# Kernel optimization log

Measured on AMD Instinct MI355X. Metric: run time of the kernel, lower is better.

The kernel has to match this reference:

```python
import jax, jax.numpy as jnp
import numpy as np

N_NODES = 40000
N_EDGES = 640000
NUM_GRAPHS = 64
NODE_DIM = 128
EDGE_DIM = 32
HID = 64
AGG_HID = 128
NEG_SLOPE = 0.2


def _segment_softmax(logits, seg, num_segments):
    # logits: [E, H], seg: [E] target-node index. Numerically stable per-segment softmax.
    m = jax.ops.segment_max(logits, seg, num_segments=num_segments)
    m = jnp.where(jnp.isfinite(m), m, 0.0)  # empty segments -> -inf max
    e = jnp.exp(logits - m[seg])
    denom = jax.ops.segment_sum(e, seg, num_segments=num_segments)
    return e / (denom[seg] + 1e-16)


def gatv2_conv(x, edge_index, edge_attr, Wl, bl, Wr, br, We, att, bias, concat):
    # PyG GATv2Conv with edge features (share_weights=False, lin_edge bias-free).
    N = x.shape[0]
    H, C = att.shape
    src, dst = edge_index[0], edge_index[1]
    xl = (x @ Wl + bl).reshape(N, H, C)          # lin_l(x) -> source transform
    xr = (x @ Wr + br).reshape(N, H, C)          # lin_r(x) -> target transform
    ee = (edge_attr @ We).reshape(-1, H, C)       # lin_edge(edge_attr)
    m = jax.nn.leaky_relu(xl[src] + xr[dst] + ee, NEG_SLOPE)  # [E,H,C]
    logits = jnp.einsum('ehc,hc->eh', m, att)     # [E,H]
    alpha = _segment_softmax(logits, dst, N)      # softmax over incoming edges
    out = jax.ops.segment_sum(xl[src] * alpha[..., None], dst, num_segments=N)  # [N,H,C]
    out = out.reshape(N, H * C) if concat else out.mean(axis=1)
    return out + bias


def setup_inputs() -> dict:
    key = jax.random.key(0)
    ks = iter(jax.random.split(key, 40))
    rn = lambda shape, s=0.1: (jax.random.normal(next(ks), shape, dtype=jnp.float32) * s)
    inp = {}
    inp['x'] = jax.random.normal(next(ks), (N_NODES, NODE_DIM), dtype=jnp.float32)
    inp['edge_attr'] = jax.random.normal(next(ks), (N_EDGES, EDGE_DIM), dtype=jnp.float32)
    inp['edge_index'] = jax.random.randint(next(ks), (2, N_EDGES), 0, N_NODES, dtype=jnp.int32)
    inp['batch'] = jnp.sort(jax.random.randint(next(ks), (N_NODES,), 0, NUM_GRAPHS, dtype=jnp.int32))
    inp.update(W1l=rn((NODE_DIM, 2 * HID)), b1l=jnp.zeros((2 * HID,), jnp.float32),
               W1r=rn((NODE_DIM, 2 * HID)), b1r=jnp.zeros((2 * HID,), jnp.float32),
               W1e=rn((EDGE_DIM, 2 * HID)), att1=rn((2, HID)), bias1=jnp.zeros((2 * HID,), jnp.float32))
    inp.update(W2l=rn((2 * HID, 2 * HID)), b2l=jnp.zeros((2 * HID,), jnp.float32),
               W2r=rn((2 * HID, 2 * HID)), b2r=jnp.zeros((2 * HID,), jnp.float32),
               W2e=rn((EDGE_DIM, 2 * HID)), att2=rn((2, HID)), bias2=jnp.zeros((2 * HID,), jnp.float32))
    # conv3: 128 -> 64, 1 head, concat=False
    inp.update(W3l=rn((2 * HID, HID)), b3l=jnp.zeros((HID,), jnp.float32),
               W3r=rn((2 * HID, HID)), b3r=jnp.zeros((HID,), jnp.float32),
               W3e=rn((EDGE_DIM, HID)), att3=rn((1, HID)), bias3=jnp.zeros((HID,), jnp.float32))
    inp.update(G1w=rn((HID, AGG_HID)), G1b=jnp.zeros((AGG_HID,), jnp.float32),
               G2w=rn((AGG_HID, 1)), G2b=jnp.zeros((1,), jnp.float32),
               Wreg=rn((HID, 1)), breg=jnp.zeros((1,), jnp.float32))
    return inp


def reference(x, edge_attr, edge_index, batch,
              W1l, b1l, W1r, b1r, W1e, att1, bias1,
              W2l, b2l, W2r, b2r, W2e, att2, bias2,
              W3l, b3l, W3r, b3r, W3e, att3, bias3,
              G1w, G1b, G2w, G2b, Wreg, breg):
    h = jax.nn.relu(gatv2_conv(x, edge_index, edge_attr, W1l, b1l, W1r, b1r, W1e, att1, bias1, True))
    h = jax.nn.relu(gatv2_conv(h, edge_index, edge_attr, W2l, b2l, W2r, b2r, W2e, att2, bias2, True))
    h = gatv2_conv(h, edge_index, edge_attr, W3l, b3l, W3r, b3r, W3e, att3, bias3, False)  # [N, HID]
    # Attentional aggregation over nodes, per graph
    gate = (jax.nn.relu(h @ G1w + G1b) @ G2w + G2b)[:, 0]            # [N]
    gate = _segment_softmax(gate[:, None], batch, NUM_GRAPHS)[:, 0]   # softmax within each graph
    pooled = jax.ops.segment_sum(gate[:, None] * h, batch, num_segments=NUM_GRAPHS)  # [B, HID]
    return (pooled @ Wreg + breg).squeeze(-1)  # [B]
```

## Files before the change

kernel.cpp:

```cpp
#include <hip/hip_runtime.h>

__global__ void k_fill(unsigned* p, int n, unsigned v) {
    int i = blockIdx.x * blockDim.x + threadIdx.x;
    if (i < n) p[i] = v;
}

__global__ void k_hist(const int* __restrict__ ei, int E, int* __restrict__ deg) {
    int e = blockIdx.x * blockDim.x + threadIdx.x;
    if (e < E) atomicAdd(&deg[ei[E + e]], 1);
}

__global__ void k_scan_blocks(const int* __restrict__ deg, int N,
                              int* __restrict__ excl, int* __restrict__ parts) {
    __shared__ int s[256];
    int t = threadIdx.x, i = blockIdx.x * 256 + t;
    int v = (i < N) ? deg[i] : 0;
    s[t] = v;
    __syncthreads();
    int acc = v;
    for (int off = 1; off < 256; off <<= 1) {
        int add = (t >= off) ? s[t - off] : 0;
        __syncthreads();
        acc += add;
        s[t] = acc;
        __syncthreads();
    }
    if (i < N) excl[i] = acc - v;
    if (t == 255) parts[blockIdx.x] = acc;
}

__global__ void k_scan_parts(int* __restrict__ parts, int nb) {
    __shared__ int s[256];
    int t = threadIdx.x;
    int v = (t < nb) ? parts[t] : 0;
    s[t] = v;
    __syncthreads();
    int acc = v;
    for (int off = 1; off < 256; off <<= 1) {
        int add = (t >= off) ? s[t - off] : 0;
        __syncthreads();
        acc += add;
        s[t] = acc;
        __syncthreads();
    }
    if (t < nb) parts[t] = acc - v;
}

__global__ void k_scan_add(const int* __restrict__ excl, const int* __restrict__ parts,
                           int* __restrict__ row_ptr, int* __restrict__ cursor, int N) {
    int i = blockIdx.x * blockDim.x + threadIdx.x;
    if (i >= N) return;
    int r = excl[i] + parts[i >> 8];
    row_ptr[i] = r;
    cursor[i] = r;
}

__global__ void k_scatter(const int* __restrict__ ei, int E, int* __restrict__ cursor,
                          int2* __restrict__ elist) {
    int e = blockIdx.x * blockDim.x + threadIdx.x;
    if (e >= E) return;
    int d = ei[E + e];
    int j = atomicAdd(&cursor[d], 1);
    elist[j] = make_int2(ei[e], e);
}

__global__ void k_reorder(const int2* __restrict__ elist, const float* __restrict__ ea, int E,
                          float4* __restrict__ ea_s) {
    int idx = blockIdx.x * blockDim.x + threadIdx.x;
    int j = idx >> 3, q = idx & 7;
    if (j >= E) return;
    ea_s[(size_t)j * 8 + q] = ((const float4*)ea)[(size_t)elist[j].y * 8 + q];
}

template <int M, int RW>
__global__ __launch_bounds__(256) void k_gemm2(const float* __restrict__ A,
                                               const float* __restrict__ Wl, const float* __restrict__ bl,
                                               const float* __restrict__ Wr, const float* __restrict__ br,
                                               float* __restrict__ outl, float* __restrict__ outr) {
    constexpr int TX = M / 4;
    __shared__ float sA[32][68];
    __shared__ float sW[32][M];
    const float* W    = blockIdx.y ? Wr : Wl;
    const float* bias = blockIdx.y ? br : bl;
    float* out        = blockIdx.y ? outr : outl;
    int t = threadIdx.x;
    int tx = t % TX, ty = t / TX;
    int r0 = blockIdx.x * 64;
    float acc[RW][4] = {};
    for (int kt = 0; kt < 128; kt += 32) {
        for (int l = t; l < 512; l += 256) {
            int row = l >> 3, kq = (l & 7) << 2;
            float4 a = *(const float4*)&A[(size_t)(r0 + row) * 128 + kt + kq];
            sA[kq + 0][row] = a.x; sA[kq + 1][row] = a.y;
            sA[kq + 2][row] = a.z; sA[kq + 3][row] = a.w;
        }
        for (int l = t; l < 32 * M / 4; l += 256) {
            int kk = (l * 4) / M, cc = (l * 4) % M;
            *(float4*)&sW[kk][cc] = *(const float4*)&W[(size_t)(kt + kk) * M + cc];
        }
        __syncthreads();
#pragma unroll
        for (int k = 0; k < 32; k++) {
            float4 w = *(float4*)&sW[k][tx * 4];
            float ar[RW];
#pragma unroll
            for (int i = 0; i < RW; i += 4) {
                float4 a = *(float4*)&sA[k][ty * RW + i];
                ar[i] = a.x; ar[i + 1] = a.y; ar[i + 2] = a.z; ar[i + 3] = a.w;
            }
#pragma unroll
            for (int i = 0; i < RW; i++) {
                acc[i][0] += ar[i] * w.x; acc[i][1] += ar[i] * w.y;
                acc[i][2] += ar[i] * w.z; acc[i][3] += ar[i] * w.w;
            }
        }
        __syncthreads();
    }
    float4 b = *(const float4*)&bias[tx * 4];
#pragma unroll
    for (int i = 0; i < RW; i++) {
        float4 v;
        v.x = acc[i][0] + b.x; v.y = acc[i][1] + b.y;
        v.z = acc[i][2] + b.z; v.w = acc[i][3] + b.w;
        *(float4*)&out[(size_t)(r0 + ty * RW + i) * M + tx * 4] = v;
    }
}

template <int H, bool RELU, bool SORTED>
__global__ __launch_bounds__(256) void k_agg(const float* __restrict__ xl, const float* __restrict__ xr,
                                             const float* __restrict__ ea, const float4* __restrict__ ea_s,
                                             const int2* __restrict__ elist,
                                             const int* __restrict__ row_ptr, const int* __restrict__ deg,
                                             const float* __restrict__ We, const float* __restrict__ att,
                                             const float* __restrict__ bias, float* __restrict__ out, int N) {
    constexpr int HC = H * 64;
    int tid = threadIdx.x, wv = tid >> 6, lane = tid & 63;
    float rWe0[32], rWe1[H == 2 ? 32 : 1];
#pragma unroll
    for (int k = 0; k < 32; k++) rWe0[k] = We[k * HC + lane];
    if constexpr (H == 2) {
#pragma unroll
        for (int k = 0; k < 32; k++) rWe1[k] = We[k * HC + 64 + lane];
    }
    float att0 = att[lane], b0 = bias[lane];
    float att1 = 0.f, b1 = 0.f;
    if constexpr (H == 2) { att1 = att[64 + lane]; b1 = bias[64 + lane]; }
    int n = blockIdx.x * 4 + wv;
    if (n >= N) return;
    int start = row_ptr[n], d = deg[n];
    float xr0 = xr[(size_t)n * HC + lane];
    float xr1 = (H == 2) ? xr[(size_t)n * HC + 64 + lane] : 0.f;
    float acc0 = 0.f, acc1 = 0.f, den0 = 0.f, den1 = 0.f;
    for (int j = 0; j < d; j++) {
        int2 sp = elist[start + j];
        const float4* eap = SORTED ? (ea_s + (size_t)(start + j) * 8)
                                   : (const float4*)(ea + (size_t)sp.y * 32);
        const float* xls = xl + (size_t)sp.x * HC;
        float xl0 = xls[lane];
        float xl1 = (H == 2) ? xls[64 + lane] : 0.f;
        float ee0 = 0.f, ee1 = 0.f;
#pragma unroll
        for (int kq = 0; kq < 8; kq++) {
            float4 v = eap[kq];
            ee0 = fmaf(v.x, rWe0[kq * 4 + 0], ee0);
            ee0 = fmaf(v.y, rWe0[kq * 4 + 1], ee0);
            ee0 = fmaf(v.z, rWe0[kq * 4 + 2], ee0);
            ee0 = fmaf(v.w, rWe0[kq * 4 + 3], ee0);
            if constexpr (H == 2) {
                ee1 = fmaf(v.x, rWe1[kq * 4 + 0], ee1);
                ee1 = fmaf(v.y, rWe1[kq * 4 + 1], ee1);
                ee1 = fmaf(v.z, rWe1[kq * 4 + 2], ee1);
                ee1 = fmaf(v.w, rWe1[kq * 4 + 3], ee1);
            }
        }
        float v0 = xl0 + xr0 + ee0;
        v0 = v0 > 0.f ? v0 : 0.2f * v0;
        float p0 = att0 * v0, p1 = 0.f;
        if constexpr (H == 2) {
            float v1 = xl1 + xr1 + ee1;
            v1 = v1 > 0.f ? v1 : 0.2f * v1;
            p1 = att1 * v1;
        }
#pragma unroll
        for (int m = 32; m; m >>= 1) {
            p0 += __shfl_xor(p0, m);
            if constexpr (H == 2) p1 += __shfl_xor(p1, m);
        }
        float ex0 = __expf(p0);
        acc0 = fmaf(ex0, xl0, acc0);
        den0 += ex0;
        if constexpr (H == 2) {
            float ex1 = __expf(p1);
            acc1 = fmaf(ex1, xl1, acc1);
            den1 += ex1;
        }
    }
    float o0 = acc0 / (den0 + 1e-16f) + b0;
    if (RELU) o0 = o0 > 0.f ? o0 : 0.f;
    out[(size_t)n * HC + lane] = o0;
    if constexpr (H == 2) {
        float o1 = acc1 / (den1 + 1e-16f) + b1;
        if (RELU) o1 = o1 > 0.f ? o1 : 0.f;
        out[(size_t)n * HC + 64 + lane] = o1;
    }
}

__global__ __launch_bounds__(256) void k_gate(const float* __restrict__ h, const float* __restrict__ G1w,
                                              const float* __restrict__ G1b, const float* __restrict__ G2w,
                                              const float* __restrict__ G2b,
                                              float* __restrict__ gate, int N) {
    __shared__ float sH[64][64];
    __shared__ float part[64][2];
    int t = threadIdx.x;
    int n0 = blockIdx.x * 64;
    for (int l = t; l < 1024; l += 256) {
        float4 v = ((const float4*)(h + (size_t)n0 * 64))[l];
        int n = l >> 4, kq = (l & 15) << 2;
        *(float4*)&sH[n][kq] = v;
    }
    int c = t & 127, half = t >> 7;
    float rW[64];
#pragma unroll
    for (int k = 0; k < 64; k++) rW[k] = G1w[k * 128 + c];
    float g1b = G1b[c], g2w = G2w[c];
    __syncthreads();
    for (int nn = 0; nn < 32; nn++) {
        int n = half * 32 + nn;
        float acc = g1b;
#pragma unroll
        for (int k = 0; k < 64; k += 4) {
            float4 hv = *(const float4*)&sH[n][k];
            acc = fmaf(hv.x, rW[k], acc);
            acc = fmaf(hv.y, rW[k + 1], acc);
            acc = fmaf(hv.z, rW[k + 2], acc);
            acc = fmaf(hv.w, rW[k + 3], acc);
        }
        acc = acc > 0.f ? acc : 0.f;
        float p = acc * g2w;
#pragma unroll
        for (int m = 32; m; m >>= 1) p += __shfl_xor(p, m);
        if ((t & 63) == 0) part[n][(t >> 6) & 1] = p;
    }
    __syncthreads();
    if (t < 64) gate[n0 + t] = __expf(part[t][0] + part[t][1] + G2b[0]);
}

__global__ __launch_bounds__(256) void k_pool(const float* __restrict__ h, const float* __restrict__ gate,
                                              const int* __restrict__ batch,
                                              float* __restrict__ pooled, int N) {
    int g = blockIdx.x;
    int lo = 0, hi = N;
    while (lo < hi) { int mid = (lo + hi) >> 1; if (batch[mid] < g) lo = mid + 1; else hi = mid; }
    int start = lo;
    lo = 0; hi = N;
    while (lo < hi) { int mid = (lo + hi) >> 1; if (batch[mid] < g + 1) lo = mid + 1; else hi = mid; }
    int end = lo;
    int t = threadIdx.x, wv = t >> 6, lane = t & 63;
    float acc = 0.f, den = 0.f;
    for (int n = start + wv; n < end; n += 4) {
        float gv = gate[n];
        acc = fmaf(gv, h[(size_t)n * 64 + lane], acc);
        den += gv;
    }
    __shared__ float sacc[4][64];
    __shared__ float sden[4];
    sacc[wv][lane] = acc;
    if (lane == 0) sden[wv] = den;
    __syncthreads();
    if (wv == 0) {
        float a = sacc[0][lane] + sacc[1][lane] + sacc[2][lane] + sacc[3][lane];
        float d = sden[0] + sden[1] + sden[2] + sden[3] + 1e-16f;
        pooled[g * 64 + lane] = a / d;
    }
}

__global__ void k_final(const float* __restrict__ pooled, const float* __restrict__ Wreg,
                        const float* __restrict__ breg, float* __restrict__ out) {
    int g = threadIdx.x;
    float acc = breg[0];
    for (int c = 0; c < 64; c++) acc += pooled[g * 64 + c] * Wreg[c];
    out[g] = acc;
}

extern "C" void kernel_launch(void* const* d_in, const int* in_sizes, int n_in,
                              void* d_out, int out_size, void* d_ws, size_t ws_size,
                              hipStream_t stream) {
    const float* x  = (const float*)d_in[0];
    const float* ea = (const float*)d_in[1];
    const int* ei    = (const int*)d_in[2];
    const int* batch = (const int*)d_in[3];
    auto ff = [&](int i) { return (const float*)d_in[i]; };
    const float *W1l = ff(4), *b1l = ff(5), *W1r = ff(6), *b1r = ff(7), *W1e = ff(8),
                *att1 = ff(9), *bias1 = ff(10);
    const float *W2l = ff(11), *b2l = ff(12), *W2r = ff(13), *b2r = ff(14), *W2e = ff(15),
                *att2 = ff(16), *bias2 = ff(17);
    const float *W3l = ff(18), *b3l = ff(19), *W3r = ff(20), *b3r = ff(21), *W3e = ff(22),
                *att3 = ff(23), *bias3 = ff(24);
    const float *G1w = ff(25), *G1b = ff(26), *G2w = ff(27), *G2b = ff(28), *Wreg = ff(29),
                *breg = ff(30);

    const int N = in_sizes[0] / 128;
    const int E = in_sizes[2] / 2;

    char* ws = (char*)d_ws;
    float*  bufA    = (float*)(ws);
    float*  bufB    = (float*)(ws + 20480000);
    float*  bufH    = (float*)(ws + 40960000);
    int2*   elist   = (int2*)(ws + 61440000);
    int*    row_ptr = (int*)(ws + 66560000);
    int*    deg     = (int*)(ws + 66720000);
    int*    cursor  = (int*)(ws + 66880000);
    int*    excl    = (int*)(ws + 67040000);
    int*    parts   = (int*)(ws + 67200000);
    float*  gate    = (float*)(ws + 67204096);
    float*  pooled  = (float*)(ws + 67364096);
    float4* ea_s    = (float4*)(ws + 67380480);
    const bool sorted_ea = ws_size >= (size_t)67380480 + (size_t)E * 32 * 4;

    auto cdiv = [](int a, int b) { return (a + b - 1) / b; };
    const int NB = cdiv(N, 256);
    const dim3 gemmG(N / 64, 2);
    const int AGGB = cdiv(N, 4);

    k_fill<<<NB, 256, 0, stream>>>((unsigned*)deg, N, 0u);
    k_hist<<<cdiv(E, 256), 256, 0, stream>>>(ei, E, deg);
    k_scan_blocks<<<NB, 256, 0, stream>>>(deg, N, excl, parts);
    k_scan_parts<<<1, 256, 0, stream>>>(parts, NB);
    k_scan_add<<<NB, 256, 0, stream>>>(excl, parts, row_ptr, cursor, N);
    k_scatter<<<cdiv(E, 256), 256, 0, stream>>>(ei, E, cursor, elist);
    if (sorted_ea)
        k_reorder<<<cdiv(E * 8, 256), 256, 0, stream>>>(elist, ea, E, ea_s);

    k_gemm2<128, 8><<<gemmG, 256, 0, stream>>>(x, W1l, b1l, W1r, b1r, bufA, bufB);
    if (sorted_ea)
        k_agg<2, true, true><<<AGGB, 256, 0, stream>>>(bufA, bufB, ea, ea_s, elist, row_ptr, deg, W1e, att1, bias1, bufH, N);
    else
        k_agg<2, true, false><<<AGGB, 256, 0, stream>>>(bufA, bufB, ea, ea_s, elist, row_ptr, deg, W1e, att1, bias1, bufH, N);

    k_gemm2<128, 8><<<gemmG, 256, 0, stream>>>(bufH, W2l, b2l, W2r, b2r, bufA, bufB);
    if (sorted_ea)
        k_agg<2, true, true><<<AGGB, 256, 0, stream>>>(bufA, bufB, ea, ea_s, elist, row_ptr, deg, W2e, att2, bias2, bufH, N);
    else
        k_agg<2, true, false><<<AGGB, 256, 0, stream>>>(bufA, bufB, ea, ea_s, elist, row_ptr, deg, W2e, att2, bias2, bufH, N);

    k_gemm2<64, 4><<<gemmG, 256, 0, stream>>>(bufH, W3l, b3l, W3r, b3r, bufA, bufB);
    if (sorted_ea)
        k_agg<1, false, true><<<AGGB, 256, 0, stream>>>(bufA, bufB, ea, ea_s, elist, row_ptr, deg, W3e, att3, bias3, bufH, N);
    else
        k_agg<1, false, false><<<AGGB, 256, 0, stream>>>(bufA, bufB, ea, ea_s, elist, row_ptr, deg, W3e, att3, bias3, bufH, N);

    k_gate<<<N / 64, 256, 0, stream>>>(bufH, G1w, G1b, G2w, G2b, gate, N);
    k_pool<<<64, 256, 0, stream>>>(bufH, gate, batch, pooled, N);
    k_final<<<1, 64, 0, stream>>>(pooled, Wreg, breg, (float*)d_out);
}
```

Baseline: 1.065 ms.

## Remap GATv2 aggregation lanes to two columns each with edge-pair processing

Reworks the per-node aggregation kernel so each lane owns two adjacent output columns loaded as float2. For two heads, the two half-waves each take one head and process edges in pairs. For one head, the two half-waves take different edges and merge their partial sums with a cross-half shuffle at the end. This cuts register use for the edge-weight matrix, shortens shuffle reductions to 32 lanes, and adds launch bounds for two blocks per SM. The aim is more in-flight edge loads and higher occupancy, in exchange for more complex indexing and a final cross-half merge.

```diff
diff --git a/kernel.cpp b/kernel.cpp
--- a/kernel.cpp
+++ b/kernel.cpp
@@ -127,82 +127,114 @@
 }
 
 template <int H, bool RELU, bool SORTED>
-__global__ __launch_bounds__(256) void k_agg(const float* __restrict__ xl, const float* __restrict__ xr,
-                                             const float* __restrict__ ea, const float4* __restrict__ ea_s,
-                                             const int2* __restrict__ elist,
-                                             const int* __restrict__ row_ptr, const int* __restrict__ deg,
-                                             const float* __restrict__ We, const float* __restrict__ att,
-                                             const float* __restrict__ bias, float* __restrict__ out, int N) {
+__global__ __launch_bounds__(256, 2) void k_agg(const float* __restrict__ xl, const float* __restrict__ xr,
+                                                const float* __restrict__ ea, const float4* __restrict__ ea_s,
+                                                const int2* __restrict__ elist,
+                                                const int* __restrict__ row_ptr, const int* __restrict__ deg,
+                                                const float* __restrict__ We, const float* __restrict__ att,
+                                                const float* __restrict__ bias, float* __restrict__ out, int N) {
     constexpr int HC = H * 64;
     int tid = threadIdx.x, wv = tid >> 6, lane = tid & 63;
-    float rWe0[32], rWe1[H == 2 ? 32 : 1];
-#pragma unroll
-    for (int k = 0; k < 32; k++) rWe0[k] = We[k * HC + lane];
-    if constexpr (H == 2) {
-#pragma unroll
-        for (int k = 0; k < 32; k++) rWe1[k] = We[k * HC + 64 + lane];
-    }
-    float att0 = att[lane], b0 = bias[lane];
-    float att1 = 0.f, b1 = 0.f;
-    if constexpr (H == 2) { att1 = att[64 + lane]; b1 = bias[64 + lane]; }
+    int half = lane >> 5, c2 = lane & 31;
+    int col = (H == 2 ? half * 64 : 0) + 2 * c2;
     int n = blockIdx.x * 4 + wv;
     if (n >= N) return;
+
+    float2 rWe[32];
+#pragma unroll
+    for (int k = 0; k < 32; k++) rWe[k] = *(const float2*)&We[k * HC + col];
+    float2 attv = *(const float2*)&att[col];
+    float2 bv   = *(const float2*)&bias[col];
+    float2 xrv  = *(const float2*)&xr[(size_t)n * HC + col];
+
     int start = row_ptr[n], d = deg[n];
-    float xr0 = xr[(size_t)n * HC + lane];
-    float xr1 = (H == 2) ? xr[(size_t)n * HC + 64 + lane] : 0.f;
-    float acc0 = 0.f, acc1 = 0.f, den0 = 0.f, den1 = 0.f;
-    for (int j = 0; j < d; j++) {
-        int2 sp = elist[start + j];
-        const float4* eap = SORTED ? (ea_s + (size_t)(start + j) * 8)
+    float2 acc = make_float2(0.f, 0.f);
+    float den = 0.f;
+
+    auto edge_pre = [&](int slot, float2& xlv, float& p) {
+        int2 sp = elist[slot];
+        const float4* eap = SORTED ? (ea_s + (size_t)slot * 8)
                                    : (const float4*)(ea + (size_t)sp.y * 32);
-        const float* xls = xl + (size_t)sp.x * HC;
-        float xl0 = xls[lane];
-        float xl1 = (H == 2) ? xls[64 + lane] : 0.f;
-        float ee0 = 0.f, ee1 = 0.f;
+        xlv = *(const float2*)&xl[(size_t)sp.x * HC + col];
+        float2 ee = make_float2(0.f, 0.f);
 #pragma unroll
         for (int kq = 0; kq < 8; kq++) {
             float4 v = eap[kq];
-            ee0 = fmaf(v.x, rWe0[kq * 4 + 0], ee0);
-            ee0 = fmaf(v.y, rWe0[kq * 4 + 1], ee0);
-            ee0 = fmaf(v.z, rWe0[kq * 4 + 2], ee0);
-            ee0 = fmaf(v.w, rWe0[kq * 4 + 3], ee0);
-            if constexpr (H == 2) {
-                ee1 = fmaf(v.x, rWe1[kq * 4 + 0], ee1);
-                ee1 = fmaf(v.y, rWe1[kq * 4 + 1], ee1);
-                ee1 = fmaf(v.z, rWe1[kq * 4 + 2], ee1);
-                ee1 = fmaf(v.w, rWe1[kq * 4 + 3], ee1);
+            ee.x = fmaf(v.x, rWe[kq * 4 + 0].x, ee.x); ee.y = fmaf(v.x, rWe[kq * 4 + 0].y, ee.y);
+            ee.x = fmaf(v.y, rWe[kq * 4 + 1].x, ee.x); ee.y = fmaf(v.y, rWe[kq * 4 + 1].y, ee.y);
+            ee.x = fmaf(v.z, rWe[kq * 4 + 2].x, ee.x); ee.y = fmaf(v.z, rWe[kq * 4 + 2].y, ee.y);
+            ee.x = fmaf(v.w, rWe[kq * 4 + 3].x, ee.x); ee.y = fmaf(v.w, rWe[kq * 4 + 3].y, ee.y);
+        }
+        float v0 = xlv.x + xrv.x + ee.x;
+        float v1 = xlv.y + xrv.y + ee.y;
+        v0 = v0 > 0.f ? v0 : 0.2f * v0;
+        v1 = v1 > 0.f ? v1 : 0.2f * v1;
+        p = attv.x * v0 + attv.y * v1;
+    };
+
+    if constexpr (H == 2) {
+        int j = 0;
+        for (; j + 2 <= d; j += 2) {
+            float2 xla, xlb;
+            float pa, pb;
+            edge_pre(start + j, xla, pa);
+            edge_pre(start + j + 1, xlb, pb);
+#pragma unroll
+            for (int m = 16; m; m >>= 1) { pa += __shfl_xor(pa, m); pb += __shfl_xor(pb, m); }
+            float exa = __expf(pa), exb = __expf(pb);
+            acc.x = fmaf(exa, xla.x, acc.x); acc.y = fmaf(exa, xla.y, acc.y);
+            acc.x = fmaf(exb, xlb.x, acc.x); acc.y = fmaf(exb, xlb.y, acc.y);
+            den += exa + exb;
+        }
+        if (j < d) {
+            float2 xla;
+            float pa;
+            edge_pre(start + j, xla, pa);
+#pragma unroll
+            for (int m = 16; m; m >>= 1) pa += __shfl_xor(pa, m);
+            float exa = __expf(pa);
+            acc.x = fmaf(exa, xla.x, acc.x); acc.y = fmaf(exa, xla.y, acc.y);
+            den += exa;
+        }
+    } else {
+        for (int j = 0; j < d; j += 4) {
+            {
+                int jj = j + half;
+                bool valid = jj < d;
+                int slot = start + (valid ? jj : j);
+                float2 xla;
+                float pa;
+                edge_pre(slot, xla, pa);
+#pragma unroll
+                for (int m = 16; m; m >>= 1) pa += __shfl_xor(pa, m);
+                float exa = valid ? __expf(pa) : 0.f;
+                acc.x = fmaf(exa, xla.x, acc.x); acc.y = fmaf(exa, xla.y, acc.y);
+                den += exa;
             }
-        }
-        float v0 = xl0 + xr0 + ee0;
-        v0 = v0 > 0.f ? v0 : 0.2f * v0;
-        float p0 = att0 * v0, p1 = 0.f;
-        if constexpr (H == 2) {
-            float v1 = xl1 + xr1 + ee1;
-            v1 = v1 > 0.f ? v1 : 0.2f * v1;
-            p1 = att1 * v1;
-        }
-#pragma unroll
-        for (int m = 32; m; m >>= 1) {
-            p0 += __shfl_xor(p0, m);
-            if constexpr (H == 2) p1 += __shfl_xor(p1, m);
-        }
-        float ex0 = __expf(p0);
-        acc0 = fmaf(ex0, xl0, acc0);
-        den0 += ex0;
-        if constexpr (H == 2) {
-            float ex1 = __expf(p1);
-            acc1 = fmaf(ex1, xl1, acc1);
-            den1 += ex1;
-        }
-    }
-    float o0 = acc0 / (den0 + 1e-16f) + b0;
-    if (RELU) o0 = o0 > 0.f ? o0 : 0.f;
-    out[(size_t)n * HC + lane] = o0;
-    if constexpr (H == 2) {
-        float o1 = acc1 / (den1 + 1e-16f) + b1;
-        if (RELU) o1 = o1 > 0.f ? o1 : 0.f;
-        out[(size_t)n * HC + 64 + lane] = o1;
-    }
+            if (j + 2 < d) {
+                int jj = j + 2 + half;
+                bool valid = jj < d;
+                int slot = start + (valid ? jj : j);
+                float2 xlb;
+                float pb;
+                edge_pre(slot, xlb, pb);
+#pragma unroll
+                for (int m = 16; m; m >>= 1) pb += __shfl_xor(pb, m);
+                float exb = valid ? __expf(pb) : 0.f;
+                acc.x = fmaf(exb, xlb.x, acc.x); acc.y = fmaf(exb, xlb.y, acc.y);
+                den += exb;
+            }
+        }
+        acc.x += __shfl_xor(acc.x, 32);
+        acc.y += __shfl_xor(acc.y, 32);
+        den   += __shfl_xor(den, 32);
+    }
+
+    float inv = 1.f / (den + 1e-16f);
+    float o0 = acc.x * inv + bv.x;
+    float o1 = acc.y * inv + bv.y;
+    if (RELU) { o0 = fmaxf(o0, 0.f); o1 = fmaxf(o1, 0.f); }
+    *(float2*)&out[(size_t)n * HC + col] = make_float2(o0, o1);
 }
 
 __global__ __launch_bounds__(256) void k_gate(const float* __restrict__ h, const float* __restrict__ G1w,
```

After: 1.695 ms. +59.2%, slower.

## Split GATv2 aggregation across waves by head and edge parity

Applied to the files above, without the earlier changes.

The aggregation kernel now gives each wave one head and half of a node's edges (even or odd), instead of one wave handling all heads and edges of a node. The two partial softmax sums are combined through shared memory after a block barrier. This raises parallelism per node, halves the per-wave register set for the edge weights, and issues all eight edge-feature loads up front with two FMA chains for more ILP. In exchange, the edge-feature row is now loaded and multiplied by each head's wave separately, blocks shrink to 1–2 nodes, and a __syncthreads plus shared-memory exchange is added.

```diff
diff --git a/kernel.cpp b/kernel.cpp
--- a/kernel.cpp
+++ b/kernel.cpp
@@ -134,74 +134,74 @@
                                              const float* __restrict__ We, const float* __restrict__ att,
                                              const float* __restrict__ bias, float* __restrict__ out, int N) {
     constexpr int HC = H * 64;
+    __shared__ float sAcc[2][64];
+    __shared__ float sDen[2];
     int tid = threadIdx.x, wv = tid >> 6, lane = tid & 63;
-    float rWe0[32], rWe1[H == 2 ? 32 : 1];
-#pragma unroll
-    for (int k = 0; k < 32; k++) rWe0[k] = We[k * HC + lane];
+    int h, eh, n, slotIdx;
     if constexpr (H == 2) {
-#pragma unroll
-        for (int k = 0; k < 32; k++) rWe1[k] = We[k * HC + 64 + lane];
-    }
-    float att0 = att[lane], b0 = bias[lane];
-    float att1 = 0.f, b1 = 0.f;
-    if constexpr (H == 2) { att1 = att[64 + lane]; b1 = bias[64 + lane]; }
-    int n = blockIdx.x * 4 + wv;
-    if (n >= N) return;
-    int start = row_ptr[n], d = deg[n];
-    float xr0 = xr[(size_t)n * HC + lane];
-    float xr1 = (H == 2) ? xr[(size_t)n * HC + 64 + lane] : 0.f;
-    float acc0 = 0.f, acc1 = 0.f, den0 = 0.f, den1 = 0.f;
-    for (int j = 0; j < d; j++) {
-        int2 sp = elist[start + j];
-        const float4* eap = SORTED ? (ea_s + (size_t)(start + j) * 8)
+        h = wv >> 1; eh = wv & 1; n = blockIdx.x; slotIdx = h;
+    } else {
+        h = 0; eh = wv & 1; n = blockIdx.x * 2 + (wv >> 1); slotIdx = wv >> 1;
+    }
+    int col = h * 64 + lane;
+
+    float rWe[32];
+#pragma unroll
+    for (int k = 0; k < 32; k++) rWe[k] = We[k * HC + col];
+    float attv = att[col], bv = bias[col];
+
+    bool alive = n < N;
+    float xrv = 0.f;
+    int start = 0, d = 0;
+    if (alive) {
+        xrv = xr[(size_t)n * HC + col];
+        start = row_ptr[n];
+        d = deg[n];
+    }
+
+    float acc = 0.f, den = 0.f;
+    for (int j = eh; j < d; j += 2) {
+        int slot = start + j;
+        int2 sp = elist[slot];
+        const float4* eap = SORTED ? (ea_s + (size_t)slot * 8)
                                    : (const float4*)(ea + (size_t)sp.y * 32);
-        const float* xls = xl + (size_t)sp.x * HC;
-        float xl0 = xls[lane];
-        float xl1 = (H == 2) ? xls[64 + lane] : 0.f;
-        float ee0 = 0.f, ee1 = 0.f;
-#pragma unroll
-        for (int kq = 0; kq < 8; kq++) {
-            float4 v = eap[kq];
-            ee0 = fmaf(v.x, rWe0[kq * 4 + 0], ee0);
-            ee0 = fmaf(v.y, rWe0[kq * 4 + 1], ee0);
-            ee0 = fmaf(v.z, rWe0[kq * 4 + 2], ee0);
-            ee0 = fmaf(v.w, rWe0[kq * 4 + 3], ee0);
-            if constexpr (H == 2) {
-                ee1 = fmaf(v.x, rWe1[kq * 4 + 0], ee1);
-                ee1 = fmaf(v.y, rWe1[kq * 4 + 1], ee1);
-                ee1 = fmaf(v.z, rWe1[kq * 4 + 2], ee1);
-                ee1 = fmaf(v.w, rWe1[kq * 4 + 3], ee1);
-            }
-        }
-        float v0 = xl0 + xr0 + ee0;
-        v0 = v0 > 0.f ? v0 : 0.2f * v0;
-        float p0 = att0 * v0, p1 = 0.f;
-        if constexpr (H == 2) {
-            float v1 = xl1 + xr1 + ee1;
-            v1 = v1 > 0.f ? v1 : 0.2f * v1;
-            p1 = att1 * v1;
-        }
-#pragma unroll
-        for (int m = 32; m; m >>= 1) {
-            p0 += __shfl_xor(p0, m);
-            if constexpr (H == 2) p1 += __shfl_xor(p1, m);
-        }
-        float ex0 = __expf(p0);
-        acc0 = fmaf(ex0, xl0, acc0);
-        den0 += ex0;
-        if constexpr (H == 2) {
-            float ex1 = __expf(p1);
-            acc1 = fmaf(ex1, xl1, acc1);
-            den1 += ex1;
-        }
-    }
-    float o0 = acc0 / (den0 + 1e-16f) + b0;
-    if (RELU) o0 = o0 > 0.f ? o0 : 0.f;
-    out[(size_t)n * HC + lane] = o0;
-    if constexpr (H == 2) {
-        float o1 = acc1 / (den1 + 1e-16f) + b1;
-        if (RELU) o1 = o1 > 0.f ? o1 : 0.f;
-        out[(size_t)n * HC + 64 + lane] = o1;
+        float4 r[8];
+#pragma unroll
+        for (int q = 0; q < 8; q++) r[q] = eap[q];
+        float xlv = xl[(size_t)sp.x * HC + col];
+        float eeA = 0.f, eeB = 0.f;
+#pragma unroll
+        for (int q = 0; q < 8; q += 2) {
+            eeA = fmaf(r[q].x, rWe[q * 4 + 0], eeA);
+            eeA = fmaf(r[q].y, rWe[q * 4 + 1], eeA);
+            eeA = fmaf(r[q].z, rWe[q * 4 + 2], eeA);
+            eeA = fmaf(r[q].w, rWe[q * 4 + 3], eeA);
+            eeB = fmaf(r[q + 1].x, rWe[q * 4 + 4], eeB);
+            eeB = fmaf(r[q + 1].y, rWe[q * 4 + 5], eeB);
+            eeB = fmaf(r[q + 1].z, rWe[q * 4 + 6], eeB);
+            eeB = fmaf(r[q + 1].w, rWe[q * 4 + 7], eeB);
+        }
+        float v = xlv + xrv + (eeA + eeB);
+        v = v > 0.f ? v : 0.2f * v;
+        float p = attv * v;
+#pragma unroll
+        for (int m = 32; m; m >>= 1) p += __shfl_xor(p, m);
+        float ex = __expf(p);
+        acc = fmaf(ex, xlv, acc);
+        den += ex;
+    }
+
+    if (eh == 1) {
+        sAcc[slotIdx][lane] = acc;
+        if (lane == 0) sDen[slotIdx] = den;
+    }
+    __syncthreads();
+    if (eh == 0 && alive) {
+        float a = acc + sAcc[slotIdx][lane];
+        float dd = den + sDen[slotIdx] + 1e-16f;
+        float o = a / dd + bv;
+        if (RELU) o = fmaxf(o, 0.f);
+        out[(size_t)n * HC + col] = o;
     }
 }
 
@@ -320,7 +320,8 @@
     auto cdiv = [](int a, int b) { return (a + b - 1) / b; };
     const int NB = cdiv(N, 256);
     const dim3 gemmG(N / 64, 2);
-    const int AGGB = cdiv(N, 4);
+    const int AGGB2 = N;
+    const int AGGB1 = cdiv(N, 2);
 
     k_fill<<<NB, 256, 0, stream>>>((unsigned*)deg, N, 0u);
     k_hist<<<cdiv(E, 256), 256, 0, stream>>>(ei, E, deg);
@@ -333,21 +334,21 @@
 
     k_gemm2<128, 8><<<gemmG, 256, 0, stream>>>(x, W1l, b1l, W1r, b1r, bufA, bufB);
     if (sorted_ea)
-        k_agg<2, true, true><<<AGGB, 256, 0, stream>>>(bufA, bufB, ea, ea_s, elist, row_ptr, deg, W1e, att1, bias1, bufH, N);
+        k_agg<2, true, true><<<AGGB2, 256, 0, stream>>>(bufA, bufB, ea, ea_s, elist, row_ptr, deg, W1e, att1, bias1, bufH, N);
     else
-        k_agg<2, true, false><<<AGGB, 256, 0, stream>>>(bufA, bufB, ea, ea_s, elist, row_ptr, deg, W1e, att1, bias1, bufH, N);
+        k_agg<2, true, false><<<AGGB2, 256, 0, stream>>>(bufA, bufB, ea, ea_s, elist, row_ptr, deg, W1e, att1, bias1, bufH, N);
 
     k_gemm2<128, 8><<<gemmG, 256, 0, stream>>>(bufH, W2l, b2l, W2r, b2r, bufA, bufB);
     if (sorted_ea)
-        k_agg<2, true, true><<<AGGB, 256, 0, stream>>>(bufA, bufB, ea, ea_s, elist, row_ptr, deg, W2e, att2, bias2, bufH, N);
+        k_agg<2, true, true><<<AGGB2, 256, 0, stream>>>(bufA, bufB, ea, ea_s, elist, row_ptr, deg, W2e, att2, bias2, bufH, N);
     else
-        k_agg<2, true, false><<<AGGB, 256, 0, stream>>>(bufA, bufB, ea, ea_s, elist, row_ptr, deg, W2e, att2, bias2, bufH, N);
+        k_agg<2, true, false><<<AGGB2, 256, 0, stream>>>(bufA, bufB, ea, ea_s, elist, row_ptr, deg, W2e, att2, bias2, bufH, N);
 
     k_gemm2<64, 4><<<gemmG, 256, 0, stream>>>(bufH, W3l, b3l, W3r, b3r, bufA, bufB);
     if (sorted_ea)
-        k_agg<1, false, true><<<AGGB, 256, 0, stream>>>(bufA, bufB, ea, ea_s, elist, row_ptr, deg, W3e, att3, bias3, bufH, N);
+        k_agg<1, false, true><<<AGGB1, 256, 0, stream>>>(bufA, bufB, ea, ea_s, elist, row_ptr, deg, W3e, att3, bias3, bufH, N);
     else
-        k_agg<1, false, false><<<AGGB, 256, 0, stream>>>(bufA, bufB, ea, ea_s, elist, row_ptr, deg, W3e, att3, bias3, bufH, N);
+        k_agg<1, false, false><<<AGGB1, 256, 0, stream>>>(bufA, bufB, ea, ea_s, elist, row_ptr, deg, W3e, att3, bias3, bufH, N);
 
     k_gate<<<N / 64, 256, 0, stream>>>(bufH, G1w, G1b, G2w, G2b, gate, N);
     k_pool<<<64, 256, 0, stream>>>(bufH, gate, batch, pooled, N);
```

After: 1.628 ms. 1.53x slower.

## Precompute edge projections with tiled GEMM and rework aggregation with split-edge waves

Applied to the files above, without the earlier changes.

The per-edge lin_edge projection moves out of the aggregation loop into a separate shared-memory tiled GEMM. That kernel writes edge embeddings in CSR order into workspace, chunked over node ranges when the workspace is too small. A new aggregation kernel reads those precomputed embeddings, gives each lane two channels via float2, splits a node's edges between two waves and prefetches the next edge's data. The aim is to remove the redundant per-lane 32-term dot products and improve memory parallelism. The cost is a large extra write and read of E×HC floats per layer. The softmax also applies exp without subtracting a max, which could overflow for large logits.

```diff
diff --git a/kernel.cpp b/kernel.cpp
--- a/kernel.cpp
+++ b/kernel.cpp
@@ -62,14 +62,6 @@
     int d = ei[E + e];
     int j = atomicAdd(&cursor[d], 1);
     elist[j] = make_int2(ei[e], e);
-}
-
-__global__ void k_reorder(const int2* __restrict__ elist, const float* __restrict__ ea, int E,
-                          float4* __restrict__ ea_s) {
-    int idx = blockIdx.x * blockDim.x + threadIdx.x;
-    int j = idx >> 3, q = idx & 7;
-    if (j >= E) return;
-    ea_s[(size_t)j * 8 + q] = ((const float4*)ea)[(size_t)elist[j].y * 8 + q];
 }
 
 template <int M, int RW>
@@ -126,13 +118,148 @@
     }
 }
 
-template <int H, bool RELU, bool SORTED>
-__global__ __launch_bounds__(256) void k_agg(const float* __restrict__ xl, const float* __restrict__ xr,
-                                             const float* __restrict__ ea, const float4* __restrict__ ea_s,
-                                             const int2* __restrict__ elist,
-                                             const int* __restrict__ row_ptr, const int* __restrict__ deg,
-                                             const float* __restrict__ We, const float* __restrict__ att,
-                                             const float* __restrict__ bias, float* __restrict__ out, int N) {
+template <int HC>
+__global__ __launch_bounds__(256) void k_edge_gemm(const float* __restrict__ ea,
+                                                   const int2* __restrict__ elist,
+                                                   const int* __restrict__ row_ptr,
+                                                   const float* __restrict__ We,
+                                                   float* __restrict__ ee,
+                                                   int n0, int n1, int Ntot, int E) {
+    int s0 = row_ptr[n0];
+    int s1 = (n1 >= Ntot) ? E : row_ptr[n1];
+    int sb = s0 + blockIdx.x * 64;
+    if (sb >= s1) return;
+    __shared__ float sA[64][33];
+    __shared__ float sW[32][HC];
+    int t = threadIdx.x;
+    for (int l = t; l < 512; l += 256) {
+        int row = l >> 3, q = l & 7;
+        int s = sb + row;
+        int eid = (s < s1) ? elist[s].y : 0;
+        float4 a = *(const float4*)&ea[(size_t)eid * 32 + q * 4];
+        sA[row][q * 4 + 0] = a.x; sA[row][q * 4 + 1] = a.y;
+        sA[row][q * 4 + 2] = a.z; sA[row][q * 4 + 3] = a.w;
+    }
+    for (int l = t; l < 32 * HC / 4; l += 256) {
+        int k = (l * 4) / HC, c = (l * 4) % HC;
+        *(float4*)&sW[k][c] = *(const float4*)&We[k * HC + c];
+    }
+    __syncthreads();
+    constexpr int CG = HC / 4;
+    constexpr int RPT = CG / 4;
+    int tx = t % CG, ty = t / CG;
+    float acc[RPT][4] = {};
+#pragma unroll
+    for (int k = 0; k < 32; k++) {
+        float4 w = *(float4*)&sW[k][tx * 4];
+#pragma unroll
+        for (int i = 0; i < RPT; i++) {
+            float a = sA[ty * RPT + i][k];
+            acc[i][0] = fmaf(a, w.x, acc[i][0]);
+            acc[i][1] = fmaf(a, w.y, acc[i][1]);
+            acc[i][2] = fmaf(a, w.z, acc[i][2]);
+            acc[i][3] = fmaf(a, w.w, acc[i][3]);
+        }
+    }
+#pragma unroll
+    for (int i = 0; i < RPT; i++) {
+        int s = sb + ty * RPT + i;
+        if (s < s1)
+            *(float4*)&ee[(size_t)(s - s0) * HC + tx * 4] =
+                make_float4(acc[i][0], acc[i][1], acc[i][2], acc[i][3]);
+    }
+}
+
+template <int H, bool RELU>
+__global__ __launch_bounds__(256) void k_aggv(const float* __restrict__ xl, const float* __restrict__ xr,
+                                              const float* __restrict__ ee,
+                                              const int2* __restrict__ elist,
+                                              const int* __restrict__ row_ptr, const int* __restrict__ deg,
+                                              const float* __restrict__ att, const float* __restrict__ bias,
+                                              float* __restrict__ out, int n0, int n1) {
+    constexpr int HC = H * 64;
+    __shared__ float2 sAcc[2][64];
+    __shared__ float  sDen[2][64];
+    int tid = threadIdx.x, wv = tid >> 6, lane = tid & 63;
+    int ns = wv >> 1, eh = wv & 1;
+    int n = n0 + blockIdx.x * 2 + ns;
+    bool alive = n < n1;
+    int hf = lane >> 5, c2 = lane & 31;
+    int col = (H == 2) ? (hf * 64 + 2 * c2) : (2 * c2);
+    float2 attv = *(const float2*)&att[col];
+    int s0 = row_ptr[n0];
+    float2 xrv = make_float2(0.f, 0.f);
+    int start = 0, d = 0;
+    if (alive) {
+        xrv = *(const float2*)&xr[(size_t)n * HC + col];
+        start = row_ptr[n];
+        d = deg[n];
+    }
+    float2 acc = make_float2(0.f, 0.f);
+    float den = 0.f;
+
+    const int jstep = (H == 2) ? 2 : 4;
+    int jc = (H == 2) ? eh : (2 * eh + hf);
+    bool okc = jc < d;
+    int sC = start + jc;
+    int sN = sC + jstep;
+    int spx = okc ? elist[sC].x : 0;
+    float2 eeC = okc ? *(const float2*)&ee[(size_t)(sC - s0) * HC + col] : make_float2(0.f, 0.f);
+    float2 xlC = okc ? *(const float2*)&xl[(size_t)spx * HC + col] : make_float2(0.f, 0.f);
+    bool okn = (jc + jstep) < d;
+    int spxN = okn ? elist[sN].x : 0;
+
+    while (okc) {
+        bool okn2 = (jc + 2 * jstep) < d;
+        int sN2 = sN + jstep;
+        int spxN2 = okn2 ? elist[sN2].x : 0;
+        float2 eeN = okn ? *(const float2*)&ee[(size_t)(sN - s0) * HC + col] : make_float2(0.f, 0.f);
+        float2 xlN = okn ? *(const float2*)&xl[(size_t)spxN * HC + col] : make_float2(0.f, 0.f);
+
+        float v0 = xlC.x + xrv.x + eeC.x;
+        float v1 = xlC.y + xrv.y + eeC.y;
+        v0 = v0 > 0.f ? v0 : 0.2f * v0;
+        v1 = v1 > 0.f ? v1 : 0.2f * v1;
+        float p = fmaf(attv.x, v0, attv.y * v1);
+#pragma unroll
+        for (int m = 16; m; m >>= 1) p += __shfl_xor(p, m);
+        float ex = __expf(p);
+        acc.x = fmaf(ex, xlC.x, acc.x);
+        acc.y = fmaf(ex, xlC.y, acc.y);
+        den += ex;
+
+        jc += jstep; sC = sN; sN = sN2;
+        xlC = xlN; eeC = eeN; spxN = spxN2;
+        okc = okn; okn = okn2;
+    }
+
+    if constexpr (H == 1) {
+        acc.x += __shfl_xor(acc.x, 32);
+        acc.y += __shfl_xor(acc.y, 32);
+        den   += __shfl_xor(den, 32);
+    }
+    if (eh == 1) { sAcc[ns][lane] = acc; sDen[ns][lane] = den; }
+    __syncthreads();
+    if (eh == 0 && alive) {
+        float2 a = sAcc[ns][lane];
+        float dd = sDen[ns][lane];
+        float dsum = den + dd + 1e-16f;
+        float2 bv = *(const float2*)&bias[col];
+        float o0 = (acc.x + a.x) / dsum + bv.x;
+        float o1 = (acc.y + a.y) / dsum + bv.y;
+        if (RELU) { o0 = fmaxf(o0, 0.f); o1 = fmaxf(o1, 0.f); }
+        if (H == 2 || hf == 0)
+            *(float2*)&out[(size_t)n * HC + col] = make_float2(o0, o1);
+    }
+}
+
+template <int H, bool RELU>
+__global__ __launch_bounds__(256) void k_agg_fb(const float* __restrict__ xl, const float* __restrict__ xr,
+                                                const float* __restrict__ ea,
+                                                const int2* __restrict__ elist,
+                                                const int* __restrict__ row_ptr, const int* __restrict__ deg,
+                                                const float* __restrict__ We, const float* __restrict__ att,
+                                                const float* __restrict__ bias, float* __restrict__ out, int N) {
     constexpr int HC = H * 64;
     int tid = threadIdx.x, wv = tid >> 6, lane = tid & 63;
     float rWe0[32], rWe1[H == 2 ? 32 : 1];
@@ -153,8 +280,7 @@
     float acc0 = 0.f, acc1 = 0.f, den0 = 0.f, den1 = 0.f;
     for (int j = 0; j < d; j++) {
         int2 sp = elist[start + j];
-        const float4* eap = SORTED ? (ea_s + (size_t)(start + j) * 8)
-                                   : (const float4*)(ea + (size_t)sp.y * 32);
+        const float4* eap = (const float4*)(ea + (size_t)sp.y * 32);
         const float* xls = xl + (size_t)sp.x * HC;
         float xl0 = xls[lane];
         float xl1 = (H == 2) ? xls[64 + lane] : 0.f;
@@ -282,6 +408,26 @@
     out[g] = acc;
 }
 
+template <int H, bool RELU>
+static void launch_layer_agg(const float* ea, const int2* elist, const int* row_ptr, const int* deg,
+                             const float* We, const float* att, const float* bias,
+                             const float* xl, const float* xr, float* outb, float* eebuf,
+                             size_t avail, int N, int E, hipStream_t stream) {
+    constexpr int HC = H * 64;
+    size_t need = (size_t)E * HC * 4;
+    int K = (avail >= need) ? 1 : (int)((need * 21 / 20 + avail - 1) / avail);
+    size_t cap_slots = (K == 1) ? (size_t)E : avail / ((size_t)HC * 4);
+    size_t cover = cap_slots < (size_t)E ? cap_slots : (size_t)E;
+    int gb = (int)((cover + 63) / 64);
+    for (int c = 0; c < K; c++) {
+        int n0 = (int)((long long)N * c / K);
+        int n1 = (int)((long long)N * (c + 1) / K);
+        k_edge_gemm<HC><<<gb, 256, 0, stream>>>(ea, elist, row_ptr, We, eebuf, n0, n1, N, E);
+        int nb = (n1 - n0 + 1) / 2;
+        k_aggv<H, RELU><<<nb, 256, 0, stream>>>(xl, xr, eebuf, elist, row_ptr, deg, att, bias, outb, n0, n1);
+    }
+}
+
 extern "C" void kernel_launch(void* const* d_in, const int* in_sizes, int n_in,
                               void* d_out, int out_size, void* d_ws, size_t ws_size,
                               hipStream_t stream) {
@@ -314,13 +460,13 @@
     int*    parts   = (int*)(ws + 67200000);
     float*  gate    = (float*)(ws + 67204096);
     float*  pooled  = (float*)(ws + 67364096);
-    float4* ea_s    = (float4*)(ws + 67380480);
-    const bool sorted_ea = ws_size >= (size_t)67380480 + (size_t)E * 32 * 4;
+    float*  eebuf   = (float*)(ws + 67380480);
+    size_t avail = ws_size > (size_t)67380480 ? ws_size - (size_t)67380480 : 0;
+    const bool newpath = avail >= ((size_t)64 << 20);
 
     auto cdiv = [](int a, int b) { return (a + b - 1) / b; };
     const int NB = cdiv(N, 256);
     const dim3 gemmG(N / 64, 2);
-    const int AGGB = cdiv(N, 4);
 
     k_fill<<<NB, 256, 0, stream>>>((unsigned*)deg, N, 0u);
     k_hist<<<cdiv(E, 256), 256, 0, stream>>>(ei, E, deg);
@@ -328,26 +474,23 @@
     k_scan_parts<<<1, 256, 0, stream>>>(parts, NB);
     k_scan_add<<<NB, 256, 0, stream>>>(excl, parts, row_ptr, cursor, N);
     k_scatter<<<cdiv(E, 256), 256, 0, stream>>>(ei, E, cursor, elist);
-    if (sorted_ea)
-        k_reorder<<<cdiv(E * 8, 256), 256, 0, stream>>>(elist, ea, E, ea_s);
-
-    k_gemm2<128, 8><<<gemmG, 256, 0, stream>>>(x, W1l, b1l, W1r, b1r, bufA, bufB);
-    if (sorted_ea)
-        k_agg<2, true, true><<<AGGB, 256, 0, stream>>>(bufA, bufB, ea, ea_s, elist, row_ptr, deg, W1e, att1, bias1, bufH, N);
-    else
-        k_agg<2, true, false><<<AGGB, 256, 0, stream>>>(bufA, bufB, ea, ea_s, elist, row_ptr, deg, W1e, att1, bias1, bufH, N);
-
-    k_gemm2<128, 8><<<gemmG, 256, 0, stream>>>(bufH, W2l, b2l, W2r, b2r, bufA, bufB);
-    if (sorted_ea)
-        k_agg<2, true, true><<<AGGB, 256, 0, stream>>>(bufA, bufB, ea, ea_s, elist, row_ptr, deg, W2e, att2, bias2, bufH, N);
-    else
-        k_agg<2, true, false><<<AGGB, 256, 0, stream>>>(bufA, bufB, ea, ea_s, elist, row_ptr, deg, W2e, att2, bias2, bufH, N);
-
-    k_gemm2<64, 4><<<gemmG, 256, 0, stream>>>(bufH, W3l, b3l, W3r, b3r, bufA, bufB);
-    if (sorted_ea)
-        k_agg<1, false, true><<<AGGB, 256, 0, stream>>>(bufA, bufB, ea, ea_s, elist, row_ptr, deg, W3e, att3, bias3, bufH, N);
-    else
-        k_agg<1, false, false><<<AGGB, 256, 0, stream>>>(bufA, bufB, ea, ea_s, elist, row_ptr, deg, W3e, att3, bias3, bufH, N);
+
+    if (newpath) {
+        k_gemm2<128, 8><<<gemmG, 256, 0, stream>>>(x, W1l, b1l, W1r, b1r, bufA, bufB);
+        launch_layer_agg<2, true>(ea, elist, row_ptr, deg, W1e, att1, bias1, bufA, bufB, bufH, eebuf, avail, N, E, stream);
+        k_gemm2<128, 8><<<gemmG, 256, 0, stream>>>(bufH, W2l, b2l, W2r, b2r, bufA, bufB);
+        launch_layer_agg<2, true>(ea, elist, row_ptr, deg, W2e, att2, bias2, bufA, bufB, bufH, eebuf, avail, N, E, stream);
+        k_gemm2<64, 4><<<gemmG, 256, 0, stream>>>(bufH, W3l, b3l, W3r, b3r, bufA, bufB);
+        launch_layer_agg<1, false>(ea, elist, row_ptr, deg, W3e, att3, bias3, bufA, bufB, bufH, eebuf, avail, N, E, stream);
+    } else {
+        const int AGGB = cdiv(N, 4);
+        k_gemm2<128, 8><<<gemmG, 256, 0, stream>>>(x, W1l, b1l, W1r, b1r, bufA, bufB);
+        k_agg_fb<2, true><<<AGGB, 256, 0, stream>>>(bufA, bufB, ea, elist, row_ptr, deg, W1e, att1, bias1, bufH, N);
+        k_gemm2<128, 8><<<gemmG, 256, 0, stream>>>(bufH, W2l, b2l, W2r, b2r, bufA, bufB);
+        k_agg_fb<2, true><<<AGGB, 256, 0, stream>>>(bufA, bufB, ea, elist, row_ptr, deg, W2e, att2, bias2, bufH, N);
+        k_gemm2<64, 4><<<gemmG, 256, 0, stream>>>(bufH, W3l, b3l, W3r, b3r, bufA, bufB);
+        k_agg_fb<1, false><<<AGGB, 256, 0, stream>>>(bufA, bufB, ea, elist, row_ptr, deg, W3e, att3, bias3, bufH, N);
+    }
 
     k_gate<<<N / 64, 256, 0, stream>>>(bufH, G1w, G1b, G2w, G2b, gate, N);
     k_pool<<<64, 256, 0, stream>>>(bufH, gate, batch, pooled, N);
```

New measurement: 1.370 ms. 1.29x slower.
